# Kernel tuning notes

Hardware: AMD Instinct MI355X
Metric: run time of the kernel (lower is better)

The kernel has to match this reference:

```python
import jax, jax.numpy as jnp
import numpy as np

B, L, D, H = 4, 2048, 1024, 16
DK = D // H  # 64


def setup_inputs() -> dict:
    key = jax.random.key(0)
    ks = jax.random.split(key, 5)
    x = jax.random.normal(ks[0], (B, L, D), dtype=jnp.float32)
    scale = 1.0 / np.sqrt(D)
    W_qkv = jax.random.normal(ks[1], (D, 3 * D), dtype=jnp.float32) * scale
    b_qkv = jnp.zeros((3 * D,), dtype=jnp.float32)
    W_out = jax.random.normal(ks[2], (D, D), dtype=jnp.float32) * scale
    b_out = jnp.zeros((D,), dtype=jnp.float32)
    return {"x": x, "W_qkv": W_qkv, "b_qkv": b_qkv, "W_out": W_out, "b_out": b_out}


def reference(x, W_qkv, b_qkv, W_out, b_out):
    Bx, Lx, Dx = x.shape
    qkv = x @ W_qkv + b_qkv                      # [B, L, 3D]
    q, k, v = jnp.split(qkv, 3, axis=-1)
    # [B, H, L, d_k]
    q = q.reshape(Bx, Lx, H, DK).transpose(0, 2, 1, 3)
    k = k.reshape(Bx, Lx, H, DK).transpose(0, 2, 1, 3)
    v = v.reshape(Bx, Lx, H, DK).transpose(0, 2, 1, 3)
    scores = jnp.einsum('bhqd,bhkd->bhqk', q, k) / np.sqrt(DK)
    causal = jnp.tril(jnp.ones((Lx, Lx), dtype=bool))
    scores = jnp.where(causal[None, None], scores, -jnp.inf)
    attn = jax.nn.softmax(scores, axis=-1)       # [B, H, L, L]
    out = jnp.einsum('bhqk,bhkd->bhqd', attn, v)
    out = out.transpose(0, 2, 1, 3).reshape(Bx, Lx, Dx)
    return out @ W_out + b_out
```

## Files before the change

### kernel.cpp

```cpp
#include <hip/hip_runtime.h>
#include <stdint.h>

#define B_ 4
#define L_ 2048
#define D_ 1024
#define H_ 16
#define DK_ 64

typedef __attribute__((ext_vector_type(8))) short bf16x8;
typedef __attribute__((ext_vector_type(4))) float f32x4;
typedef unsigned short bfu;

#define MFMA(a, b, c) __builtin_amdgcn_mfma_f32_16x16x32_bf16((a), (b), (c), 0, 0, 0)

__device__ __forceinline__ unsigned short f2bf(float f) {
  union { float f; unsigned int u; } v; v.f = f;
  unsigned int u = v.u;
  return (unsigned short)((u + 0x7fffu + ((u >> 16) & 1u)) >> 16);
}

__device__ __forceinline__ void gll16(const void* g, void* l) {
  __builtin_amdgcn_global_load_lds(
      (const __attribute__((address_space(1))) void*)g,
      (__attribute__((address_space(3))) void*)l, 16, 0, 0);
}

#define VMCNT(n_) asm volatile("s_waitcnt vmcnt(" #n_ ")" ::: "memory")
#define BARRIER() asm volatile("s_barrier" ::: "memory")


__global__ __launch_bounds__(256) void cast_x(const float* __restrict__ in,
                                              bfu* __restrict__ out, int n4) {
  int i = blockIdx.x * 256 + threadIdx.x;
  if (i >= n4) return;
  float4 v = ((const float4*)in)[i];
  ushort4 o;
  o.x = f2bf(v.x); o.y = f2bf(v.y); o.z = f2bf(v.z); o.w = f2bf(v.w);
  ((ushort4*)out)[i] = o;
}

__global__ __launch_bounds__(256) void wpack(const float* __restrict__ in,
                                             bfu* __restrict__ out, int K, int C) {
  int idx = blockIdx.x * 256 + threadIdx.x;
  if (idx >= K * C) return;
  int k = idx / C, c = idx % C;
  size_t o = ((size_t)(c >> 4) * (K >> 3) + (k >> 3)) * 128 + (c & 15) * 8 + (k & 7);
  out[o] = f2bf(in[idx]);
}


template <int EPI>
__global__ __launch_bounds__(256, 2) void gemm_r(
    const bfu* __restrict__ A, const bfu* __restrict__ Bp,
    const float* __restrict__ bias, bfu* __restrict__ Qg, bfu* __restrict__ Kg,
    bfu* __restrict__ Vtg, float* __restrict__ Out, int M, int N, int K) {
  __shared__ __align__(16) bfu As[2][128 * 64];
  const int tid = threadIdx.x;
  const int lane = tid & 63;
  const int w = tid >> 6;
  const int wm = w >> 1, wn = w & 1;
  const int l15 = lane & 15, l4 = lane >> 4;

  const int nwg = gridDim.x;
  const int cpx = nwg >> 3;
  const int bid = (int)blockIdx.x;
  const int swz = (bid & 7) * cpx + (bid >> 3);
  const int NTt = N / 128;
  const int m0 = ((swz & 7) + 8 * (swz / (8 * NTt))) * 128;
  const int n0 = ((swz >> 3) % NTt) * 128;
  const int K8 = K >> 3;

  auto stageA = [&](int t) {
    char* lb = (char*)As[t & 1];
#pragma unroll
    for (int j = 0; j < 4; ++j) {
      int idx = j * 256 + tid;
      int row = idx >> 3, c16p = idx & 7, c16 = c16p ^ (row & 7);
      gll16(A + (size_t)(m0 + row) * K + t * 64 + c16 * 8,
            lb + row * 128 + c16p * 16);
    }
  };

  const size_t bbase = ((size_t)((n0 + wn * 64) >> 4)) * K8;
  auto loadB = [&](int t, bf16x8 (&br)[4][2]) {
#pragma unroll
    for (int ni = 0; ni < 4; ++ni)
#pragma unroll
      for (int kk = 0; kk < 2; ++kk)
        br[ni][kk] = *(const bf16x8*)(
            Bp + (bbase + (size_t)ni * K8 + t * 8 + kk * 4 + l4) * 128 + l15 * 8);
  };

  f32x4 acc[4][4] = {};
  bf16x8 af[4][2], brA[4][2], brB[4][2];

  auto lda = [&](int t) {
    const char* base = (const char*)As[t & 1];
#pragma unroll
    for (int mi = 0; mi < 4; ++mi)
#pragma unroll
      for (int kk = 0; kk < 2; ++kk) {
        int row = wm * 64 + mi * 16 + l15;
        int ch = (kk * 4 + l4) ^ (row & 7);
        af[mi][kk] = *(const bf16x8*)(base + row * 128 + ch * 16);
      }
  };
  auto mm_all = [&](bf16x8 (&br)[4][2]) {
    __builtin_amdgcn_s_setprio(1);
#pragma unroll
    for (int kk = 0; kk < 2; ++kk)
#pragma unroll
      for (int mi = 0; mi < 4; ++mi)
#pragma unroll
        for (int ni = 0; ni < 4; ++ni)
          acc[mi][ni] = MFMA(af[mi][kk], br[ni][kk], acc[mi][ni]);
    __builtin_amdgcn_s_setprio(0);
  };

  const int NT = K >> 6;
  stageA(0);
  __builtin_amdgcn_sched_barrier(0);
  loadB(0, brA);
  loadB(1, brB);

  for (int t = 0; t < NT; t += 2) {
    VMCNT(8); BARRIER();
    lda(t);
    stageA(t + 1);
    __builtin_amdgcn_sched_barrier(0);
    mm_all(brA);
    if (t + 2 < NT) loadB(t + 2, brA);
    if (t + 2 < NT) { VMCNT(8); } else { VMCNT(0); }
    BARRIER();
    lda(t + 1);
    if (t + 2 < NT) stageA(t + 2);
    __builtin_amdgcn_sched_barrier(0);
    mm_all(brB);
    if (t + 3 < NT) loadB(t + 3, brB);
  }

  if constexpr (EPI == 1) {
#pragma unroll
    for (int ni = 0; ni < 4; ++ni) {
      int gn = n0 + wn * 64 + ni * 16 + l15;
      float bv = bias[gn];
#pragma unroll
      for (int mi = 0; mi < 4; ++mi)
#pragma unroll
        for (int rg = 0; rg < 4; ++rg) {
          int gm = m0 + wm * 64 + mi * 16 + l4 * 4 + rg;
          Out[(size_t)gm * N + gn] = acc[mi][ni][rg] + bv;
        }
    }
  } else {
    const int sec = n0 >> 10;
    if (sec < 2) {
      bfu* dst = (sec == 0) ? Qg : Kg;
      const float scale = (sec == 0) ? 0.18033688011112042f : 1.0f;
#pragma unroll
      for (int ni = 0; ni < 4; ++ni) {
        int gn = n0 + wn * 64 + ni * 16 + l15;
        int rem = gn & 1023;
        int hh = rem >> 6, dk = rem & 63;
        float bv = bias[gn];
#pragma unroll
        for (int mi = 0; mi < 4; ++mi)
#pragma unroll
          for (int rg = 0; rg < 4; ++rg) {
            int gm = m0 + wm * 64 + mi * 16 + l4 * 4 + rg;
            int bb = gm >> 11, ll = gm & 2047;
            dst[(((size_t)(bb * H_ + hh)) * L_ + ll) * DK_ + dk] =
                f2bf((acc[mi][ni][rg] + bv) * scale);
          }
      }
    } else {
      __syncthreads();
#pragma unroll
      for (int ni = 0; ni < 4; ++ni) {
        int n_local = wn * 64 + ni * 16 + l15;
        int gn = n0 + n_local;
        float bv = bias[gn];
        int swzn = (n_local & 7) << 4;
#pragma unroll
        for (int mi = 0; mi < 4; ++mi) {
          int m_base = wm * 64 + mi * 16 + l4 * 4;
          int k6 = m_base & 63;
          int p0 = (m_base & ~63) |
                   ((k6 & 32) | (((k6 >> 2) & 3) << 3) | (((k6 >> 4) & 1) << 2));
          float v0 = acc[mi][ni][0] + bv, v1 = acc[mi][ni][1] + bv;
          float v2 = acc[mi][ni][2] + bv, v3 = acc[mi][ni][3] + bv;
          uint32_t w01, w23;
          asm("v_cvt_pk_bf16_f32 %0, %1, %2" : "=v"(w01) : "v"(v0), "v"(v1));
          asm("v_cvt_pk_bf16_f32 %0, %1, %2" : "=v"(w23) : "v"(v2), "v"(v3));
          *(uint32_t*)((char*)As + n_local * 256 + ((2 * p0) ^ swzn)) = w01;
          *(uint32_t*)((char*)As + n_local * 256 + ((2 * p0 + 4) ^ swzn)) = w23;
        }
      }
      __syncthreads();
      int n = tid >> 1;
      int cb = (tid & 1) * 8;
      int gnn = n0 + n;
      int hh = (gnn >> 6) & 15, dk = gnn & 63;
      size_t rowbase =
          (((size_t)((m0 >> 11) * H_ + hh)) * DK_ + dk) * L_ + (m0 & 2047);
#pragma unroll
      for (int j = 0; j < 8; ++j) {
        int ch = cb + j;
        bf16x8 vv = *(const bf16x8*)((char*)As + n * 256 +
                                     ((ch * 16) ^ ((n & 7) << 4)));
        *(bf16x8*)(Vtg + rowbase + ch * 8) = vv;
      }
    }
  }
}


__global__ __launch_bounds__(256, 3) void attn(const bfu* __restrict__ Qg,
                                               const bfu* __restrict__ Kg,
                                               const bfu* __restrict__ Vtg,
                                               bfu* __restrict__ Ao) {
  __shared__ __align__(16) bfu Ks[2 * 64 * 64];
  __shared__ __align__(16) bfu Vs[2 * 64 * 64];

  const int tid = threadIdx.x;
  const int lane = tid & 63;
  const int w = tid >> 6;
  const int l15 = lane & 15, l4 = lane >> 4;

  const int hid = blockIdx.x;
  const int xcd = hid & 7, slot = hid >> 3;
  const int bh = xcd * 8 + (slot >> 3);
  const int p = slot & 7;
  const int b = bh >> 4, h = bh & 15;

  for (int seg = 0; seg < 2; ++seg) {
    const int qb = (seg == 0) ? p : 15 - p;
    const int q0 = qb * 128;
    const int nt = 2 * qb + 2;
    const int q0w = q0 + w * 32;

    bf16x8 qf[2][2];
#pragma unroll
    for (int mi = 0; mi < 2; ++mi)
#pragma unroll
      for (int kk = 0; kk < 2; ++kk)
        qf[mi][kk] = *(const bf16x8*)(
            Qg + ((size_t)bh * L_ + q0w + mi * 16 + l15) * DK_ + kk * 32 + l4 * 8);

#pragma unroll
    for (int i = 0; i < 2; ++i) {
      int lb = i * 256 + tid;
      int r = lb >> 3, c16 = (lb & 7) ^ (r & 7);
      gll16(Kg + ((size_t)bh * L_ + r) * DK_ + c16 * 8, (char*)Ks + lb * 16);
      gll16(Vtg + ((size_t)bh * DK_ + r) * L_ + c16 * 8, (char*)Vs + lb * 16);
    }
    VMCNT(0);
    BARRIER();

    f32x4 acco[2][4] = {};
    float m[2] = {-1e30f, -1e30f};
    float l[2] = {0.f, 0.f};

    for (int t = 0; t < nt; ++t) {
      const int cur = t & 1;
      const int kv0 = t * 64;
      const char* Kc = (const char*)Ks + cur * 8192;
      const char* Vc = (const char*)Vs + cur * 8192;

      if (t + 1 < nt) {
        const int nb = (t + 1) & 1, nkv = (t + 1) * 64;
#pragma unroll
        for (int i = 0; i < 2; ++i) {
          int lb = i * 256 + tid;
          int r = lb >> 3, c16 = (lb & 7) ^ (r & 7);
          gll16(Kg + ((size_t)bh * L_ + nkv + r) * DK_ + c16 * 8,
                (char*)Ks + nb * 8192 + lb * 16);
          gll16(Vtg + ((size_t)bh * DK_ + r) * L_ + nkv + c16 * 8,
                (char*)Vs + nb * 8192 + lb * 16);
        }
        VMCNT(4);
      } else {
        VMCNT(0);
      }
      BARRIER();

      if (kv0 <= q0w + 31) {
        f32x4 s[2][4] = {};
        __builtin_amdgcn_s_setprio(1);
#pragma unroll
        for (int kk = 0; kk < 2; ++kk)
#pragma unroll
          for (int ni = 0; ni < 4; ++ni) {
            int r = ni * 16 + l15;
            int ch = (kk * 4 + l4) ^ (r & 7);
            bf16x8 kf = *(const bf16x8*)(Kc + r * 128 + ch * 16);
#pragma unroll
            for (int mi = 0; mi < 2; ++mi)
              s[mi][ni] = MFMA(kf, qf[mi][kk], s[mi][ni]);
          }
        __builtin_amdgcn_s_setprio(0);

        if (kv0 + 63 > q0w) {
#pragma unroll
          for (int mi = 0; mi < 2; ++mi) {
            int qg_ = q0w + mi * 16 + l15;
#pragma unroll
            for (int ni = 0; ni < 4; ++ni) {
              int kvg = kv0 + ni * 16 + l4 * 4;
#pragma unroll
              for (int rg = 0; rg < 4; ++rg)
                if (kvg + rg > qg_) s[mi][ni][rg] = -1e30f;
            }
          }
        }

        float mx[2];
#pragma unroll
        for (int mi = 0; mi < 2; ++mi) {
          float v = fmaxf(fmaxf(fmaxf(s[mi][0][0], s[mi][0][1]),
                                fmaxf(s[mi][0][2], s[mi][0][3])),
                          fmaxf(fmaxf(s[mi][1][0], s[mi][1][1]),
                                fmaxf(s[mi][1][2], s[mi][1][3])));
          v = fmaxf(v, fmaxf(fmaxf(fmaxf(s[mi][2][0], s[mi][2][1]),
                                   fmaxf(s[mi][2][2], s[mi][2][3])),
                             fmaxf(fmaxf(s[mi][3][0], s[mi][3][1]),
                                   fmaxf(s[mi][3][2], s[mi][3][3]))));
          v = fmaxf(v, __shfl_xor(v, 16));
          v = fmaxf(v, __shfl_xor(v, 32));
          mx[mi] = v;
        }
        float grow = fmaxf(mx[0] - m[0], mx[1] - m[1]);
        if (__any(grow > 11.0f)) {
#pragma unroll
          for (int mi = 0; mi < 2; ++mi) {
            float mn = fmaxf(m[mi], mx[mi]);
            float sc = __builtin_amdgcn_exp2f(m[mi] - mn);
            m[mi] = mn;
            l[mi] *= sc;
#pragma unroll
            for (int rg = 0; rg < 4; ++rg) {
              float scq = __shfl(sc, l4 * 4 + rg);
              acco[mi][0][rg] *= scq; acco[mi][1][rg] *= scq;
              acco[mi][2][rg] *= scq; acco[mi][3][rg] *= scq;
            }
          }
        }

        uint32_t pk[2][4][2];
#pragma unroll
        for (int mi = 0; mi < 2; ++mi)
#pragma unroll
          for (int ni = 0; ni < 4; ++ni) {
            float p0 = __builtin_amdgcn_exp2f(s[mi][ni][0] - m[mi]);
            float p1 = __builtin_amdgcn_exp2f(s[mi][ni][1] - m[mi]);
            float p2 = __builtin_amdgcn_exp2f(s[mi][ni][2] - m[mi]);
            float p3 = __builtin_amdgcn_exp2f(s[mi][ni][3] - m[mi]);
            l[mi] += (p0 + p1) + (p2 + p3);
            asm("v_cvt_pk_bf16_f32 %0, %1, %2" : "=v"(pk[mi][ni][0]) : "v"(p0), "v"(p1));
            asm("v_cvt_pk_bf16_f32 %0, %1, %2" : "=v"(pk[mi][ni][1]) : "v"(p2), "v"(p3));
          }

        __builtin_amdgcn_s_setprio(1);
#pragma unroll
        for (int kk = 0; kk < 2; ++kk) {
          union { uint32_t wd[4]; bf16x8 v; } u[2];
#pragma unroll
          for (int mi = 0; mi < 2; ++mi) {
            u[mi].wd[0] = pk[mi][2 * kk][0];
            u[mi].wd[1] = pk[mi][2 * kk][1];
            u[mi].wd[2] = pk[mi][2 * kk + 1][0];
            u[mi].wd[3] = pk[mi][2 * kk + 1][1];
          }
#pragma unroll
          for (int ni = 0; ni < 4; ++ni) {
            int r = ni * 16 + l15;
            int ch = (kk * 4 + l4) ^ (r & 7);
            bf16x8 vf = *(const bf16x8*)(Vc + r * 128 + ch * 16);
#pragma unroll
            for (int mi = 0; mi < 2; ++mi)
              acco[mi][ni] = MFMA(u[mi].v, vf, acco[mi][ni]);
          }
        }
        __builtin_amdgcn_s_setprio(0);
      }

      BARRIER();
    }

#pragma unroll
    for (int mi = 0; mi < 2; ++mi) {
      float ls = l[mi];
      ls += __shfl_xor(ls, 16);
      ls += __shfl_xor(ls, 32);
      float linv = 1.0f / ls;
#pragma unroll
      for (int rg = 0; rg < 4; ++rg) {
        float lq = __shfl(linv, l4 * 4 + rg);
        int q = q0w + mi * 16 + l4 * 4 + rg;
#pragma unroll
        for (int ni = 0; ni < 4; ++ni) {
          int d = ni * 16 + l15;
          Ao[((size_t)b * L_ + q) * D_ + h * DK_ + d] = f2bf(acco[mi][ni][rg] * lq);
        }
      }
    }
  }
}


extern "C" void kernel_launch(void* const* d_in, const int* in_sizes, int n_in,
                              void* d_out, int out_size, void* d_ws, size_t ws_size,
                              hipStream_t stream) {
  const float* x = (const float*)d_in[0];
  const float* W_qkv = (const float*)d_in[1];
  const float* b_qkv = (const float*)d_in[2];
  const float* W_out = (const float*)d_in[3];
  const float* b_out = (const float*)d_in[4];
  float* out = (float*)d_out;

  char* ws = (char*)d_ws;
  bfu* xb     = (bfu*)(ws);
  bfu* Wqkv_p = (bfu*)(ws + 16777216);
  bfu* Wout_p = (bfu*)(ws + 23068672);
  bfu* Qg     = (bfu*)(ws + 25165824);
  bfu* Kg     = (bfu*)(ws + 41943040);
  bfu* Vtg    = (bfu*)(ws + 58720256);
  bfu* Ao     = (bfu*)(ws + 75497472);

  cast_x<<<8192, 256, 0, stream>>>(x, xb, 2097152);
  wpack<<<12288, 256, 0, stream>>>(W_qkv, Wqkv_p, 1024, 3072);
  wpack<<<4096, 256, 0, stream>>>(W_out, Wout_p, 1024, 1024);

  gemm_r<0><<<1536, 256, 0, stream>>>(xb, Wqkv_p, b_qkv, Qg, Kg, Vtg, nullptr,
                                      8192, 3072, 1024);
  attn<<<512, 256, 0, stream>>>(Qg, Kg, Vtg, Ao);
  gemm_r<1><<<512, 256, 0, stream>>>(Ao, Wout_p, b_out, nullptr, nullptr, nullptr,
                                     out, 8192, 1024, 1024);
}
```

Before: 163.9 us.

## Widen QKV GEMM tile to 128x256 and vectorize weight packing

```diff
diff --git a/kernel.cpp b/kernel.cpp
--- a/kernel.cpp
+++ b/kernel.cpp
@@ -39,13 +39,168 @@
   ((ushort4*)out)[i] = o;
 }
 
-__global__ __launch_bounds__(256) void wpack(const float* __restrict__ in,
-                                             bfu* __restrict__ out, int K, int C) {
+__global__ __launch_bounds__(256) void wpack2(const float* __restrict__ in,
+                                              bfu* __restrict__ out, int K, int C) {
   int idx = blockIdx.x * 256 + threadIdx.x;
-  if (idx >= K * C) return;
-  int k = idx / C, c = idx % C;
-  size_t o = ((size_t)(c >> 4) * (K >> 3) + (k >> 3)) * 128 + (c & 15) * 8 + (k & 7);
-  out[o] = f2bf(in[idx]);
+  int c = idx % C, kb = idx / C;
+  if (kb >= (K >> 3)) return;
+  unsigned short v[8];
+#pragma unroll
+  for (int j = 0; j < 8; ++j) v[j] = f2bf(in[(size_t)(kb * 8 + j) * C + c]);
+  size_t o = ((size_t)(c >> 4) * (K >> 3) + kb) * 128 + (c & 15) * 8;
+  *(ushort4*)(out + o) = make_ushort4(v[0], v[1], v[2], v[3]);
+  *(ushort4*)(out + o + 4) = make_ushort4(v[4], v[5], v[6], v[7]);
+}
+
+
+__global__ __launch_bounds__(256, 2) void gemm_n(
+    const bfu* __restrict__ A, const bfu* __restrict__ Bp,
+    const float* __restrict__ bias, bfu* __restrict__ Qg, bfu* __restrict__ Kg,
+    bfu* __restrict__ Vtg, int M, int N, int K) {
+  __shared__ __align__(16) bfu As[2][128 * 64];
+  const int tid = threadIdx.x;
+  const int lane = tid & 63;
+  const int w = tid >> 6;
+  const int wm = w >> 1, wn = w & 1;
+  const int l15 = lane & 15, l4 = lane >> 4;
+
+  const int nwg = gridDim.x;
+  const int cpx = nwg >> 3;
+  const int bid = (int)blockIdx.x;
+  const int swz = (bid & 7) * cpx + (bid >> 3);
+  const int NTt = N / 256;
+  const int m0 = ((swz & 7) + 8 * (swz / (8 * NTt))) * 128;
+  const int n0 = ((swz >> 3) % NTt) * 256;
+  const int K8 = K >> 3;
+
+  auto stageA = [&](int t) {
+    char* lb = (char*)As[t & 1];
+#pragma unroll
+    for (int j = 0; j < 4; ++j) {
+      int idx = j * 256 + tid;
+      int row = idx >> 3, c16p = idx & 7, c16 = c16p ^ (row & 7);
+      gll16(A + (size_t)(m0 + row) * K + t * 64 + c16 * 8,
+            lb + row * 128 + c16p * 16);
+    }
+  };
+
+  const size_t bbase = ((size_t)((n0 + wn * 128) >> 4)) * K8;
+  auto loadB = [&](int t, int h, bf16x8 (&br)[4][2]) {
+#pragma unroll
+    for (int ni = 0; ni < 4; ++ni)
+#pragma unroll
+      for (int kk = 0; kk < 2; ++kk)
+        br[ni][kk] = *(const bf16x8*)(
+            Bp + (bbase + (size_t)(h * 4 + ni) * K8 + t * 8 + kk * 4 + l4) * 128 +
+            l15 * 8);
+  };
+
+  f32x4 acc[4][8] = {};
+  bf16x8 af[4][2], brX[4][2], brY[4][2];
+
+  auto lda = [&](int t) {
+    const char* base = (const char*)As[t & 1];
+#pragma unroll
+    for (int mi = 0; mi < 4; ++mi)
+#pragma unroll
+      for (int kk = 0; kk < 2; ++kk) {
+        int row = wm * 64 + mi * 16 + l15;
+        int ch = (kk * 4 + l4) ^ (row & 7);
+        af[mi][kk] = *(const bf16x8*)(base + row * 128 + ch * 16);
+      }
+  };
+  auto mm_half = [&](bf16x8 (&br)[4][2], int h) {
+    __builtin_amdgcn_s_setprio(1);
+#pragma unroll
+    for (int kk = 0; kk < 2; ++kk)
+#pragma unroll
+      for (int mi = 0; mi < 4; ++mi)
+#pragma unroll
+        for (int ni = 0; ni < 4; ++ni)
+          acc[mi][h * 4 + ni] = MFMA(af[mi][kk], br[ni][kk], acc[mi][h * 4 + ni]);
+    __builtin_amdgcn_s_setprio(0);
+  };
+
+  const int NT = K >> 6;
+  stageA(0);
+  __builtin_amdgcn_sched_barrier(0);
+  loadB(0, 0, brX);
+
+  for (int t = 0; t < NT; ++t) {
+    VMCNT(0); BARRIER();
+    lda(t);
+    loadB(t, 1, brY);
+    if (t + 1 < NT) stageA(t + 1);
+    __builtin_amdgcn_sched_barrier(0);
+    mm_half(brX, 0);
+    if (t + 1 < NT) loadB(t + 1, 0, brX);
+    mm_half(brY, 1);
+  }
+
+  const int sec = n0 >> 10;
+  if (sec < 2) {
+    bfu* dst = (sec == 0) ? Qg : Kg;
+    const float scale = (sec == 0) ? 0.18033688011112042f : 1.0f;
+#pragma unroll
+    for (int ni = 0; ni < 8; ++ni) {
+      int gn = n0 + wn * 128 + ni * 16 + l15;
+      int rem = gn & 1023;
+      int hh = rem >> 6, dk = rem & 63;
+      float bv = bias[gn];
+#pragma unroll
+      for (int mi = 0; mi < 4; ++mi)
+#pragma unroll
+        for (int rg = 0; rg < 4; ++rg) {
+          int gm = m0 + wm * 64 + mi * 16 + l4 * 4 + rg;
+          int bb = gm >> 11, ll = gm & 2047;
+          dst[(((size_t)(bb * H_ + hh)) * L_ + ll) * DK_ + dk] =
+              f2bf((acc[mi][ni][rg] + bv) * scale);
+        }
+    }
+  } else {
+    __syncthreads();
+#pragma unroll
+    for (int p = 0; p < 2; ++p) {
+      if (wn == p) {
+#pragma unroll
+        for (int ni = 0; ni < 8; ++ni) {
+          int n_rel = ni * 16 + l15;
+          int gn = n0 + p * 128 + n_rel;
+          float bv = bias[gn];
+          int swzn = (n_rel & 7) << 4;
+#pragma unroll
+          for (int mi = 0; mi < 4; ++mi) {
+            int m_base = wm * 64 + mi * 16 + l4 * 4;
+            int k6 = m_base & 63;
+            int p0 = (m_base & ~63) |
+                     ((k6 & 32) | (((k6 >> 2) & 3) << 3) | (((k6 >> 4) & 1) << 2));
+            float v0 = acc[mi][ni][0] + bv, v1 = acc[mi][ni][1] + bv;
+            float v2 = acc[mi][ni][2] + bv, v3 = acc[mi][ni][3] + bv;
+            uint32_t w01, w23;
+            asm("v_cvt_pk_bf16_f32 %0, %1, %2" : "=v"(w01) : "v"(v0), "v"(v1));
+            asm("v_cvt_pk_bf16_f32 %0, %1, %2" : "=v"(w23) : "v"(v2), "v"(v3));
+            *(uint32_t*)((char*)As + n_rel * 256 + ((2 * p0) ^ swzn)) = w01;
+            *(uint32_t*)((char*)As + n_rel * 256 + ((2 * p0 + 4) ^ swzn)) = w23;
+          }
+        }
+      }
+      __syncthreads();
+      int n = tid >> 1;
+      int cb = (tid & 1) * 8;
+      int gnn = n0 + p * 128 + n;
+      int hh = (gnn >> 6) & 15, dk = gnn & 63;
+      size_t rowbase =
+          (((size_t)((m0 >> 11) * H_ + hh)) * DK_ + dk) * L_ + (m0 & 2047);
+#pragma unroll
+      for (int j = 0; j < 8; ++j) {
+        int ch = cb + j;
+        bf16x8 vv = *(const bf16x8*)((char*)As + n * 256 +
+                                     ((ch * 16) ^ ((n & 7) << 4)));
+        *(bf16x8*)(Vtg + rowbase + ch * 8) = vv;
+      }
+      __syncthreads();
+    }
+  }
 }
 
 
@@ -152,65 +307,6 @@
           Out[(size_t)gm * N + gn] = acc[mi][ni][rg] + bv;
         }
     }
-  } else {
-    const int sec = n0 >> 10;
-    if (sec < 2) {
-      bfu* dst = (sec == 0) ? Qg : Kg;
-      const float scale = (sec == 0) ? 0.18033688011112042f : 1.0f;
-#pragma unroll
-      for (int ni = 0; ni < 4; ++ni) {
-        int gn = n0 + wn * 64 + ni * 16 + l15;
-        int rem = gn & 1023;
-        int hh = rem >> 6, dk = rem & 63;
-        float bv = bias[gn];
-#pragma unroll
-        for (int mi = 0; mi < 4; ++mi)
-#pragma unroll
-          for (int rg = 0; rg < 4; ++rg) {
-            int gm = m0 + wm * 64 + mi * 16 + l4 * 4 + rg;
-            int bb = gm >> 11, ll = gm & 2047;
-            dst[(((size_t)(bb * H_ + hh)) * L_ + ll) * DK_ + dk] =
-                f2bf((acc[mi][ni][rg] + bv) * scale);
-          }
-      }
-    } else {
-      __syncthreads();
-#pragma unroll
-      for (int ni = 0; ni < 4; ++ni) {
-        int n_local = wn * 64 + ni * 16 + l15;
-        int gn = n0 + n_local;
-        float bv = bias[gn];
-        int swzn = (n_local & 7) << 4;
-#pragma unroll
-        for (int mi = 0; mi < 4; ++mi) {
-          int m_base = wm * 64 + mi * 16 + l4 * 4;
-          int k6 = m_base & 63;
-          int p0 = (m_base & ~63) |
-                   ((k6 & 32) | (((k6 >> 2) & 3) << 3) | (((k6 >> 4) & 1) << 2));
-          float v0 = acc[mi][ni][0] + bv, v1 = acc[mi][ni][1] + bv;
-          float v2 = acc[mi][ni][2] + bv, v3 = acc[mi][ni][3] + bv;
-          uint32_t w01, w23;
-          asm("v_cvt_pk_bf16_f32 %0, %1, %2" : "=v"(w01) : "v"(v0), "v"(v1));
-          asm("v_cvt_pk_bf16_f32 %0, %1, %2" : "=v"(w23) : "v"(v2), "v"(v3));
-          *(uint32_t*)((char*)As + n_local * 256 + ((2 * p0) ^ swzn)) = w01;
-          *(uint32_t*)((char*)As + n_local * 256 + ((2 * p0 + 4) ^ swzn)) = w23;
-        }
-      }
-      __syncthreads();
-      int n = tid >> 1;
-      int cb = (tid & 1) * 8;
-      int gnn = n0 + n;
-      int hh = (gnn >> 6) & 15, dk = gnn & 63;
-      size_t rowbase =
-          (((size_t)((m0 >> 11) * H_ + hh)) * DK_ + dk) * L_ + (m0 & 2047);
-#pragma unroll
-      for (int j = 0; j < 8; ++j) {
-        int ch = cb + j;
-        bf16x8 vv = *(const bf16x8*)((char*)As + n * 256 +
-                                     ((ch * 16) ^ ((n & 7) << 4)));
-        *(bf16x8*)(Vtg + rowbase + ch * 8) = vv;
-      }
-    }
   }
 }
 
@@ -428,11 +524,10 @@
   bfu* Ao     = (bfu*)(ws + 75497472);
 
   cast_x<<<8192, 256, 0, stream>>>(x, xb, 2097152);
-  wpack<<<12288, 256, 0, stream>>>(W_qkv, Wqkv_p, 1024, 3072);
-  wpack<<<4096, 256, 0, stream>>>(W_out, Wout_p, 1024, 1024);
-
-  gemm_r<0><<<1536, 256, 0, stream>>>(xb, Wqkv_p, b_qkv, Qg, Kg, Vtg, nullptr,
-                                      8192, 3072, 1024);
+  wpack2<<<1536, 256, 0, stream>>>(W_qkv, Wqkv_p, 1024, 3072);
+  wpack2<<<512, 256, 0, stream>>>(W_out, Wout_p, 1024, 1024);
+
+  gemm_n<<<768, 256, 0, stream>>>(xb, Wqkv_p, b_qkv, Qg, Kg, Vtg, 8192, 3072, 1024);
   attn<<<512, 256, 0, stream>>>(Qg, Kg, Vtg, Ao);
   gemm_r<1><<<512, 256, 0, stream>>>(Ao, Wout_p, b_out, nullptr, nullptr, nullptr,
                                      out, 8192, 1024, 1024);
```

After: 161.0 us. No clear change (-1.8%).
